# Kernel optimization log

Hardware: AMD Instinct MI355X
Metric: run time of the kernel (lower is better)

Reference implementation:

```python
import jax, jax.numpy as jnp
import numpy as np

B, C, O, H, W, K, KS = 32, 128, 128, 56, 56, 4, 3
EPS = 1e-5


def setup_inputs() -> dict:
    key = jax.random.key(0)
    ks = jax.random.split(key, 6)
    sc = lambda k, shape, s: jax.random.normal(k, shape, jnp.float32) * s
    return {
        "x": jax.random.normal(ks[0], (B, C, H, W), jnp.float32),
        "fc1_w": sc(ks[1], (K, C), 0.05),
        "fc1_b": jnp.zeros((K,), jnp.float32),
        "fc2_w": sc(ks[2], (K, K), 0.3),
        "fc2_b": jnp.zeros((K,), jnp.float32),
        "weight": sc(ks[3], (K, O, C, KS, KS), 0.05),  # [K, out, in/groups, kh, kw]
        "bias": sc(ks[4], (K, O), 0.05),
        "gamma": jnp.ones((O,), jnp.float32),
        "beta": jnp.zeros((O,), jnp.float32),
    }


def reference(x, fc1_w, fc1_b, fc2_w, fc2_b, weight, bias, gamma, beta):
    # attention2d: global avg pool -> 1x1 conv (== linear) -> relu -> 1x1 conv -> softmax over K
    pooled = x.mean(axis=(2, 3))                          # [B, C]
    h = jax.nn.relu(pooled @ fc1_w.T + fc1_b)             # [B, K]
    attn = jax.nn.softmax(h @ fc2_w.T + fc2_b, axis=-1)   # [B, K]

    # per-sample aggregated kernel / bias
    agg_w = jnp.einsum('bk,koihw->boihw', attn, weight)   # [B, O, C, KS, KS]
    agg_b = attn @ bias                                    # [B, O]

    # per-sample conv (== groups=batch trick in torch)
    def conv_one(xi, wi):
        return jax.lax.conv_general_dilated(
            xi[None], wi, window_strides=(1, 1),
            padding=((1, 1), (1, 1)),
            dimension_numbers=('NCHW', 'OIHW', 'NCHW'))[0]

    out = jax.vmap(conv_one)(x, agg_w) + agg_b[:, :, None, None]  # [B, O, H, W]

    # BatchNorm2d in training mode: biased batch stats over (N, H, W)
    mean = out.mean(axis=(0, 2, 3))
    var = out.var(axis=(0, 2, 3))
    out = (out - mean[None, :, None, None]) * jax.lax.rsqrt(var + EPS)[None, :, None, None]
    out = out * gamma[None, :, None, None] + beta[None, :, None, None]
    return jax.nn.relu(out)
```

## Files before the change

### kernel.cpp

```cpp
#include <hip/hip_runtime.h>
#include <hip/hip_bf16.h>

#define BB 32
#define CC 128
#define OO 128
#define HH 56
#define WW 56
#define KK 4
#define HW 3136
#define WPLANE 147456
#define EPSV 1e-5f

#define NPOS 348
#define BUFB 22528

typedef __attribute__((ext_vector_type(8))) short short8v;
typedef __attribute__((ext_vector_type(4))) float f32x4;

static __device__ __forceinline__ void gload16(const void* g, void* l) {
    __builtin_amdgcn_global_load_lds((const __attribute__((address_space(1))) void*)g,
                                     (__attribute__((address_space(3))) void*)l, 16, 0, 0);
}

__global__ void convert_pool_kernel(const float* __restrict__ x,
                                    ushort* __restrict__ xbf,
                                    float* __restrict__ pooledp,
                                    ushort* __restrict__ zpage) {
    const int h = blockIdx.x, b = blockIdx.y;
    if (h == 0 && b == 0 && threadIdx.x < 32) zpage[threadIdx.x] = 0;
    __shared__ float4 xl4[1792];
    const float* xp = x + (size_t)(b * CC) * HW + h * WW;

    #pragma unroll
    for (int k = 0; k < 7; ++k) {
        int u = threadIdx.x + k * 256;
        int c = u / 14, w4 = u - c * 14;
        float4 v = *(const float4*)(xp + (size_t)c * HW + w4 * 4);
        xl4[u ^ ((c >> 3) & 7)] = v;
    }
    __syncthreads();

    const float* xf = (const float*)xl4;
    #pragma unroll
    for (int k = 0; k < 4; ++k) {
        int v = threadIdx.x + k * 256;
        if (v < 896) {
            int w = v >> 4, c8 = v & 15;
            int w4 = w >> 2, wo = w & 3;
            short8v res;
            #pragma unroll
            for (int j = 0; j < 8; ++j) {
                int c = c8 * 8 + j;
                int su = (c * 14 + w4) ^ (c8 & 7);
                __hip_bfloat16 hb = __float2bfloat16(xf[su * 4 + wo]);
                res[j] = *(short*)&hb;
            }
            *(short8v*)(xbf + ((size_t)((b * HH + h) * WW + w)) * CC + c8 * 8) = res;
        }
    }

    if (threadIdx.x < 128) {
        int c = threadIdx.x;
        float s = 0.f;
        #pragma unroll
        for (int w4 = 0; w4 < 14; ++w4) {
            float4 v = xl4[(c * 14 + w4) ^ ((c >> 3) & 7)];
            s += v.x + v.y + v.z + v.w;
        }
        pooledp[((size_t)(b * HH + h)) * CC + c] = s;
    }
}

__global__ void attn_kernel(const float* __restrict__ pooledp,
                            const float* __restrict__ fc1_w, const float* __restrict__ fc1_b,
                            const float* __restrict__ fc2_w, const float* __restrict__ fc2_b,
                            float* __restrict__ attn) {
    const int b = blockIdx.x, c = threadIdx.x;
    float s = 0.f;
    for (int h = 0; h < HH; ++h) s += pooledp[((size_t)(b * HH + h)) * CC + c];
    const float pc = s * (1.0f / HW);
    __shared__ float red[8];
    const int lane = c & 63, wid = c >> 6;
    #pragma unroll
    for (int k = 0; k < KK; ++k) {
        float v = pc * fc1_w[k * CC + c];
        for (int off = 32; off > 0; off >>= 1) v += __shfl_down(v, off, 64);
        if (lane == 0) red[k * 2 + wid] = v;
    }
    __syncthreads();
    if (c == 0) {
        float hk[KK], z[KK], m = -1e30f, den = 0.f;
        #pragma unroll
        for (int k = 0; k < KK; ++k)
            hk[k] = fmaxf(red[k * 2] + red[k * 2 + 1] + fc1_b[k], 0.f);
        #pragma unroll
        for (int k = 0; k < KK; ++k) {
            float t = fc2_b[k];
            #pragma unroll
            for (int j = 0; j < KK; ++j) t += hk[j] * fc2_w[k * KK + j];
            z[k] = t; m = fmaxf(m, t);
        }
        #pragma unroll
        for (int k = 0; k < KK; ++k) { z[k] = expf(z[k] - m); den += z[k]; }
        #pragma unroll
        for (int k = 0; k < KK; ++k) attn[b * KK + k] = z[k] / den;
    }
}

__global__ void aggw_kernel(const float* __restrict__ attn, const float* __restrict__ weight,
                            const float* __restrict__ bias,
                            ushort* __restrict__ aggw, float* __restrict__ agg_b) {
    int idx = blockIdx.x * 256 + threadIdx.x;
    if (idx < BB * 9 * OO * CC) {
        int cc = idx & 31;
        int t1 = idx >> 5;
        int o  = t1 & 127;
        int t2 = t1 >> 7;
        int ci = t2 & 3;
        int t3 = t2 >> 2;
        int j  = t3 % 9;
        int b  = t3 / 9;
        int c  = ci * 32 + cc;
        size_t wi = ((size_t)(o * CC + c)) * 9 + j;
        float s = attn[b*KK + 0] * weight[wi]
                + attn[b*KK + 1] * weight[wi + (size_t)WPLANE]
                + attn[b*KK + 2] * weight[wi + (size_t)2*WPLANE]
                + attn[b*KK + 3] * weight[wi + (size_t)3*WPLANE];
        __hip_bfloat16 hb = __float2bfloat16(s);
        aggw[idx] = *(ushort*)&hb;
    }
    if (blockIdx.x < 16) {
        int i = blockIdx.x * 256 + threadIdx.x;
        int b = i >> 7, o = i & 127;
        float s = 0.f;
        #pragma unroll
        for (int k = 0; k < KK; ++k) s += attn[b*KK + k] * bias[k*OO + o];
        agg_b[i] = s;
    }
}

static __device__ __forceinline__ void conv_body(
        const ushort* __restrict__ xbf, const ushort* __restrict__ aggw,
        const ushort* __restrict__ zpage, ushort* xs,
        int b, int h0, int wg, int wy, int cf, int kg, int wid, int lane,
        f32x4 (&acc)[4][7]) {
    const ushort* gp[6]; int gstep[6];
    #pragma unroll
    for (int k = 0; k < 6; ++k) {
        int q = wid + 4 * k;
        int un = q * 64 + lane;
        int u = un ^ ((un >> 3) & 7);
        int pos = u >> 2, quad = u & 3;
        int row = pos / 58, col = pos - row * 58;
        int gh = h0 - 1 + row, gw = col - 1;
        bool valid = (pos < NPOS) && (gh >= 0) && (gh < HH) && (gw >= 0) && (gw < WW);
        gp[k] = valid ? (xbf + ((size_t)((b * HH + gh) * WW + gw)) * CC + quad * 8) : zpage;
        gstep[k] = valid ? 32 : 0;
    }

    int blin[7];
    #pragma unroll
    for (int nf = 0; nf < 7; ++nf) {
        int p = wy * 112 + nf * 16 + cf;
        int r = p / 56, w = p - r * 56;
        blin[nf] = (((r + 1) * 58 + (w + 1)) << 6) + kg * 16;
    }

    const ushort* Ab = aggw + ((size_t)b * 36) * 4096 + (size_t)(wg * 64 + cf) * 32 + kg * 8;
    #define ALOAD(mf_, j_, ci_) (*(const short8v*)(Ab + (size_t)((j_) * 4 + (ci_)) * 4096 + (mf_) * 512))

    short8v pa[4];
    #pragma unroll
    for (int mf = 0; mf < 4; ++mf) pa[mf] = ALOAD(mf, 0, 0);

    #pragma unroll
    for (int k = 0; k < 6; ++k) {
        int q = wid + 4 * k;
        if (q < 22) { gload16(gp[k], (char*)xs + q * 1024); gp[k] += gstep[k]; }
    }
    __syncthreads();

    int cur = 0;
    for (int ci = 0; ci < 4; ++ci) {
        if (ci < 3) {
            char* base = (char*)xs + (cur ^ 1) * BUFB;
            #pragma unroll
            for (int k = 0; k < 6; ++k) {
                int q = wid + 4 * k;
                if (q < 22) { gload16(gp[k], base + q * 1024); gp[k] += gstep[k]; }
            }
        }
        const char* xbuf = (const char*)xs + cur * BUFB;

        short8v bfc[7], bfn[7];
        #pragma unroll
        for (int nf = 0; nf < 7; ++nf) {
            int lin = blin[nf] + (-58 - 1) * 64;
            int swz = lin ^ ((lin >> 3) & 0x70);
            bfc[nf] = *(const short8v*)(xbuf + swz);
        }
        #pragma unroll
        for (int j = 0; j < 9; ++j) {
            if (j < 8) {
                const int toff = (((j+1)/3 - 1) * 58 + ((j+1)%3 - 1)) * 64;
                #pragma unroll
                for (int nf = 0; nf < 7; ++nf) {
                    int lin = blin[nf] + toff;
                    int swz = lin ^ ((lin >> 3) & 0x70);
                    bfn[nf] = *(const short8v*)(xbuf + swz);
                }
            }
            short8v ca[4];
            #pragma unroll
            for (int mf = 0; mf < 4; ++mf) ca[mf] = pa[mf];
            if (j < 8) {
                #pragma unroll
                for (int mf = 0; mf < 4; ++mf) pa[mf] = ALOAD(mf, j + 1, ci);
            } else if (ci < 3) {
                #pragma unroll
                for (int mf = 0; mf < 4; ++mf) pa[mf] = ALOAD(mf, 0, ci + 1);
            }
            #pragma unroll
            for (int nf = 0; nf < 7; ++nf) {
                #pragma unroll
                for (int mf = 0; mf < 4; ++mf)
                    acc[mf][nf] = __builtin_amdgcn_mfma_f32_16x16x32_bf16(ca[mf], bfc[nf], acc[mf][nf], 0, 0, 0);
            }
            if (j < 8) {
                #pragma unroll
                for (int nf = 0; nf < 7; ++nf) bfc[nf] = bfn[nf];
            }
        }
        if (ci < 3) __syncthreads();
        cur ^= 1;
    }
    #undef ALOAD
}

template <bool BF16OUT>
__launch_bounds__(256, 2)
__global__ void conv_kernel(const ushort* __restrict__ xbf, const ushort* __restrict__ aggw,
                            const float* __restrict__ agg_b, const ushort* __restrict__ zpage,
                            void* __restrict__ outv,
                            float* __restrict__ psum, float* __restrict__ psumsq) {
    const int lid  = blockIdx.x;
    const int gwid = (lid & 7) * 56 + (lid >> 3);
    const int b = gwid / 14;
    const int t = gwid - b * 14;
    const int h0 = t * 4;
    __shared__ ushort xs[2 * BUFB / 2];

    const int tid  = threadIdx.x;
    const int lane = tid & 63;
    const int wid  = tid >> 6;
    const int wg = wid & 1, wy = wid >> 1;
    const int cf = lane & 15, kg = lane >> 4;

    f32x4 acc[4][7];
    #pragma unroll
    for (int mf = 0; mf < 4; ++mf)
        #pragma unroll
        for (int nf = 0; nf < 7; ++nf) acc[mf][nf] = (f32x4){0.f, 0.f, 0.f, 0.f};

    conv_body(xbf, aggw, zpage, xs, b, h0, wg, wy, cf, kg, wid, lane, acc);

    #pragma unroll
    for (int mf = 0; mf < 4; ++mf) {
        #pragma unroll
        for (int i = 0; i < 4; ++i) {
            const int o = wg * 64 + mf * 16 + kg * 4 + i;
            const float ab = agg_b[b * OO + o];
            const size_t obase = ((size_t)(b * OO + o)) * HW;
            float s = 0.f, s2 = 0.f;
            #pragma unroll
            for (int nf = 0; nf < 7; ++nf) {
                int p = wy * 112 + nf * 16 + cf;
                int r = p / 56, w = p - r * 56;
                float v = acc[mf][nf][i] + ab;
                if (BF16OUT) {
                    __hip_bfloat16 hb = __float2bfloat16(v);
                    ((ushort*)outv)[obase + (h0 + r) * WW + w] = *(ushort*)&hb;
                } else {
                    ((float*)outv)[obase + (h0 + r) * WW + w] = v;
                }
                s += v; s2 += v * v;
            }
            s  += __shfl_xor(s, 1, 64);  s  += __shfl_xor(s, 2, 64);
            s  += __shfl_xor(s, 4, 64);  s  += __shfl_xor(s, 8, 64);
            s2 += __shfl_xor(s2, 1, 64); s2 += __shfl_xor(s2, 2, 64);
            s2 += __shfl_xor(s2, 4, 64); s2 += __shfl_xor(s2, 8, 64);
            if (cf == 0) {
                int row = (b * 14 + t) * 2 + wy;
                psum[row * OO + o]   = s;
                psumsq[row * OO + o] = s2;
            }
        }
    }
}

__global__ void finstats_kernel(const float* __restrict__ psum, const float* __restrict__ psumsq,
                                float* __restrict__ sums, float* __restrict__ sumsq) {
    const int o = blockIdx.x, l = threadIdx.x;
    float s = 0.f, s2 = 0.f;
    for (int r = l; r < 896; r += 64) { s += psum[r * OO + o]; s2 += psumsq[r * OO + o]; }
    for (int off = 32; off > 0; off >>= 1) {
        s  += __shfl_down(s, off, 64);
        s2 += __shfl_down(s2, off, 64);
    }
    if (l == 0) { sums[o] = s; sumsq[o] = s2; }
}

__global__ void bn_bf16_kernel(const ushort* __restrict__ convout, float* __restrict__ out,
                               const float* __restrict__ sums, const float* __restrict__ sumsq,
                               const float* __restrict__ gamma, const float* __restrict__ beta) {
    const float invN = 1.0f / (float)(BB * HW);
    const int total8 = BB * OO * HW / 8;
    for (int i = blockIdx.x * blockDim.x + threadIdx.x; i < total8; i += gridDim.x * blockDim.x) {
        int o = (i / (HW/8)) % OO;
        float mean = sums[o] * invN;
        float var  = sumsq[o] * invN - mean*mean;
        float inv  = rsqrtf(var + EPSV);
        float g  = gamma[o] * inv;
        float bt = beta[o] - mean * g;
        short8v v = *(const short8v*)(convout + (size_t)i * 8);
        float4 lo, hi;
        #pragma unroll
        for (int j = 0; j < 4; ++j) {
            ushort u = (ushort)v[j];
            float f = __bfloat162float(*(__hip_bfloat16*)&u);
            ((float*)&lo)[j] = fmaxf(f * g + bt, 0.f);
        }
        #pragma unroll
        for (int j = 0; j < 4; ++j) {
            ushort u = (ushort)v[4 + j];
            float f = __bfloat162float(*(__hip_bfloat16*)&u);
            ((float*)&hi)[j] = fmaxf(f * g + bt, 0.f);
        }
        ((float4*)out)[i * 2]     = lo;
        ((float4*)out)[i * 2 + 1] = hi;
    }
}

__global__ void bn_kernel(float* __restrict__ out,
                          const float* __restrict__ sums, const float* __restrict__ sumsq,
                          const float* __restrict__ gamma, const float* __restrict__ beta) {
    const float invN = 1.0f / (float)(BB * HW);
    const int total4 = BB * OO * HW / 4;
    for (int i = blockIdx.x * blockDim.x + threadIdx.x; i < total4; i += gridDim.x * blockDim.x) {
        int o = (i / (HW/4)) % OO;
        float mean = sums[o] * invN;
        float var  = sumsq[o] * invN - mean*mean;
        float inv  = rsqrtf(var + EPSV);
        float g  = gamma[o] * inv;
        float bt = beta[o] - mean * g;
        float4 v = ((float4*)out)[i];
        v.x = fmaxf(v.x*g + bt, 0.f);
        v.y = fmaxf(v.y*g + bt, 0.f);
        v.z = fmaxf(v.z*g + bt, 0.f);
        v.w = fmaxf(v.w*g + bt, 0.f);
        ((float4*)out)[i] = v;
    }
}

extern "C" void kernel_launch(void* const* d_in, const int* in_sizes, int n_in,
                              void* d_out, int out_size, void* d_ws, size_t ws_size,
                              hipStream_t stream) {
    const float* x      = (const float*)d_in[0];
    const float* fc1_w  = (const float*)d_in[1];
    const float* fc1_b  = (const float*)d_in[2];
    const float* fc2_w  = (const float*)d_in[3];
    const float* fc2_b  = (const float*)d_in[4];
    const float* weight = (const float*)d_in[5];
    const float* bias   = (const float*)d_in[6];
    const float* gamma  = (const float*)d_in[7];
    const float* beta   = (const float*)d_in[8];
    float* out = (float*)d_out;

    const size_t XBF_ELEMS  = (size_t)BB * HW * CC;
    const size_t AGGW_ELEMS = (size_t)BB * 9 * OO * CC;
    const size_t OUT_ELEMS  = (size_t)BB * OO * HW;
    ushort* xbf  = (ushort*)d_ws;
    ushort* aggw = xbf + XBF_ELEMS;
    float*  wsf  = (float*)(aggw + AGGW_ELEMS);
    float* pooledp = wsf;
    float* attn    = pooledp + 229376;
    float* agg_b   = attn + 128;
    float* psum    = agg_b + 4096;
    float* psumsq  = psum + 114688;
    float* sums    = psumsq + 114688;
    float* sumsq   = sums + 128;
    ushort* zpage  = (ushort*)(sumsq + 128);
    ushort* convout = (ushort*)(zpage + 32);

    const size_t need = (size_t)((char*)(convout + OUT_ELEMS) - (char*)d_ws);
    const bool bf16path = ws_size >= need;

    convert_pool_kernel<<<dim3(HH, BB), 256, 0, stream>>>(x, xbf, pooledp, zpage);
    attn_kernel<<<BB, 128, 0, stream>>>(pooledp, fc1_w, fc1_b, fc2_w, fc2_b, attn);
    aggw_kernel<<<(int)((AGGW_ELEMS + 255)/256), 256, 0, stream>>>(attn, weight, bias, aggw, agg_b);

    if (bf16path) {
        conv_kernel<true><<<dim3(448), 256, 0, stream>>>(xbf, aggw, agg_b, zpage,
                                                         (void*)convout, psum, psumsq);
        finstats_kernel<<<OO, 64, 0, stream>>>(psum, psumsq, sums, sumsq);
        bn_bf16_kernel<<<2048, 256, 0, stream>>>(convout, out, sums, sumsq, gamma, beta);
    } else {
        conv_kernel<false><<<dim3(448), 256, 0, stream>>>(xbf, aggw, agg_b, zpage,
                                                          (void*)out, psum, psumsq);
        finstats_kernel<<<OO, 64, 0, stream>>>(psum, psumsq, sums, sumsq);
        bn_kernel<<<2048, 256, 0, stream>>>(out, sums, sumsq, gamma, beta);
    }
}
```

Baseline: 99.77 us.

## Fuse attention into aggw, fold BN stats into apply kernel, deepen weight prefetch

Merges the attention MLP kernel into the aggregated-weight kernel, so every block recomputes the per-sample attention from the pooled partial sums. The stats-finalise kernel is merged into a per-channel BN apply kernel, and the partial sums are transposed to a channel-major layout so each block reads them contiguously. The conv inner loop now prefetches aggregated-weight fragments two taps ahead instead of one. Together these remove two kernel launches and hide more global latency, at the cost of redundant attention and stats reductions per block and more registers in the conv kernel.

```diff
diff --git a/kernel.cpp b/kernel.cpp
--- a/kernel.cpp
+++ b/kernel.cpp
@@ -71,24 +71,35 @@
     }
 }
 
-__global__ void attn_kernel(const float* __restrict__ pooledp,
-                            const float* __restrict__ fc1_w, const float* __restrict__ fc1_b,
-                            const float* __restrict__ fc2_w, const float* __restrict__ fc2_b,
-                            float* __restrict__ attn) {
-    const int b = blockIdx.x, c = threadIdx.x;
-    float s = 0.f;
-    for (int h = 0; h < HH; ++h) s += pooledp[((size_t)(b * HH + h)) * CC + c];
-    const float pc = s * (1.0f / HW);
+__global__ void attn_aggw_kernel(const float* __restrict__ pooledp,
+                                 const float* __restrict__ fc1_w, const float* __restrict__ fc1_b,
+                                 const float* __restrict__ fc2_w, const float* __restrict__ fc2_b,
+                                 const float* __restrict__ weight, const float* __restrict__ bias,
+                                 ushort* __restrict__ aggw, float* __restrict__ agg_b) {
+    const int b   = blockIdx.x / 36;
+    const int rem = blockIdx.x % 36;
+    const int j   = rem >> 2;
+    const int ci  = rem & 3;
+
     __shared__ float red[8];
-    const int lane = c & 63, wid = c >> 6;
-    #pragma unroll
-    for (int k = 0; k < KK; ++k) {
-        float v = pc * fc1_w[k * CC + c];
-        for (int off = 32; off > 0; off >>= 1) v += __shfl_down(v, off, 64);
-        if (lane == 0) red[k * 2 + wid] = v;
-    }
-    __syncthreads();
-    if (c == 0) {
+    __shared__ float att[4];
+    const int tid = threadIdx.x;
+    const int lane = tid & 63, wv = tid >> 6;
+
+    if (tid < 128) {
+        const int c = tid;
+        float s = 0.f;
+        for (int h = 0; h < HH; ++h) s += pooledp[((size_t)(b * HH + h)) * CC + c];
+        const float pc = s * (1.0f / HW);
+        #pragma unroll
+        for (int k = 0; k < KK; ++k) {
+            float v = pc * fc1_w[k * CC + c];
+            for (int off = 32; off > 0; off >>= 1) v += __shfl_down(v, off, 64);
+            if (lane == 0) red[k * 2 + wv] = v;
+        }
+    }
+    __syncthreads();
+    if (tid == 0) {
         float hk[KK], z[KK], m = -1e30f, den = 0.f;
         #pragma unroll
         for (int k = 0; k < KK; ++k)
@@ -97,45 +108,38 @@
         for (int k = 0; k < KK; ++k) {
             float t = fc2_b[k];
             #pragma unroll
-            for (int j = 0; j < KK; ++j) t += hk[j] * fc2_w[k * KK + j];
+            for (int jj = 0; jj < KK; ++jj) t += hk[jj] * fc2_w[k * KK + jj];
             z[k] = t; m = fmaxf(m, t);
         }
         #pragma unroll
         for (int k = 0; k < KK; ++k) { z[k] = expf(z[k] - m); den += z[k]; }
         #pragma unroll
-        for (int k = 0; k < KK; ++k) attn[b * KK + k] = z[k] / den;
-    }
-}
-
-__global__ void aggw_kernel(const float* __restrict__ attn, const float* __restrict__ weight,
-                            const float* __restrict__ bias,
-                            ushort* __restrict__ aggw, float* __restrict__ agg_b) {
-    int idx = blockIdx.x * 256 + threadIdx.x;
-    if (idx < BB * 9 * OO * CC) {
-        int cc = idx & 31;
-        int t1 = idx >> 5;
-        int o  = t1 & 127;
-        int t2 = t1 >> 7;
-        int ci = t2 & 3;
-        int t3 = t2 >> 2;
-        int j  = t3 % 9;
-        int b  = t3 / 9;
-        int c  = ci * 32 + cc;
+        for (int k = 0; k < KK; ++k) att[k] = z[k] / den;
+    }
+    __syncthreads();
+    const float a0 = att[0], a1 = att[1], a2 = att[2], a3 = att[3];
+
+    if (rem == 0 && tid < 128) {
+        const int o = tid;
+        float s = 0.f;
+        #pragma unroll
+        for (int k = 0; k < KK; ++k) s += att[k] * bias[k * OO + o];
+        agg_b[b * OO + o] = s;
+    }
+
+    ushort* op = aggw + (((size_t)b * 9 + j) * 4 + ci) * 4096;
+    #pragma unroll 4
+    for (int it = 0; it < 16; ++it) {
+        int idx2 = tid + it * 256;
+        int cc = idx2 & 31, o = idx2 >> 5;
+        int c = ci * 32 + cc;
         size_t wi = ((size_t)(o * CC + c)) * 9 + j;
-        float s = attn[b*KK + 0] * weight[wi]
-                + attn[b*KK + 1] * weight[wi + (size_t)WPLANE]
-                + attn[b*KK + 2] * weight[wi + (size_t)2*WPLANE]
-                + attn[b*KK + 3] * weight[wi + (size_t)3*WPLANE];
+        float s = a0 * weight[wi]
+                + a1 * weight[wi + (size_t)WPLANE]
+                + a2 * weight[wi + (size_t)2*WPLANE]
+                + a3 * weight[wi + (size_t)3*WPLANE];
         __hip_bfloat16 hb = __float2bfloat16(s);
-        aggw[idx] = *(ushort*)&hb;
-    }
-    if (blockIdx.x < 16) {
-        int i = blockIdx.x * 256 + threadIdx.x;
-        int b = i >> 7, o = i & 127;
-        float s = 0.f;
-        #pragma unroll
-        for (int k = 0; k < KK; ++k) s += attn[b*KK + k] * bias[k*OO + o];
-        agg_b[i] = s;
+        op[idx2] = *(ushort*)&hb;
     }
 }
 
@@ -169,9 +173,11 @@
     const ushort* Ab = aggw + ((size_t)b * 36) * 4096 + (size_t)(wg * 64 + cf) * 32 + kg * 8;
     #define ALOAD(mf_, j_, ci_) (*(const short8v*)(Ab + (size_t)((j_) * 4 + (ci_)) * 4096 + (mf_) * 512))
 
-    short8v pa[4];
-    #pragma unroll
-    for (int mf = 0; mf < 4; ++mf) pa[mf] = ALOAD(mf, 0, 0);
+    short8v paA[4], paB[4];
+    #pragma unroll
+    for (int mf = 0; mf < 4; ++mf) paA[mf] = ALOAD(mf, 0, 0);
+    #pragma unroll
+    for (int mf = 0; mf < 4; ++mf) paB[mf] = ALOAD(mf, 1, 0);
 
     #pragma unroll
     for (int k = 0; k < 6; ++k) {
@@ -212,13 +218,14 @@
             }
             short8v ca[4];
             #pragma unroll
-            for (int mf = 0; mf < 4; ++mf) ca[mf] = pa[mf];
-            if (j < 8) {
-                #pragma unroll
-                for (int mf = 0; mf < 4; ++mf) pa[mf] = ALOAD(mf, j + 1, ci);
+            for (int mf = 0; mf < 4; ++mf) { ca[mf] = paA[mf]; paA[mf] = paB[mf]; }
+            const int f = j + 2;
+            if (f < 9) {
+                #pragma unroll
+                for (int mf = 0; mf < 4; ++mf) paB[mf] = ALOAD(mf, f, ci);
             } else if (ci < 3) {
                 #pragma unroll
-                for (int mf = 0; mf < 4; ++mf) pa[mf] = ALOAD(mf, 0, ci + 1);
+                for (int mf = 0; mf < 4; ++mf) paB[mf] = ALOAD(mf, f - 9, ci + 1);
             }
             #pragma unroll
             for (int nf = 0; nf < 7; ++nf) {
@@ -291,74 +298,77 @@
             s2 += __shfl_xor(s2, 4, 64); s2 += __shfl_xor(s2, 8, 64);
             if (cf == 0) {
                 int row = (b * 14 + t) * 2 + wy;
-                psum[row * OO + o]   = s;
-                psumsq[row * OO + o] = s2;
-            }
-        }
-    }
-}
-
-__global__ void finstats_kernel(const float* __restrict__ psum, const float* __restrict__ psumsq,
-                                float* __restrict__ sums, float* __restrict__ sumsq) {
-    const int o = blockIdx.x, l = threadIdx.x;
+                psum[o * 896 + row]   = s;
+                psumsq[o * 896 + row] = s2;
+            }
+        }
+    }
+}
+
+template <bool BF16IN>
+__global__ void bn2_kernel(const void* __restrict__ src, float* __restrict__ out,
+                           const float* __restrict__ psum, const float* __restrict__ psumsq,
+                           const float* __restrict__ gamma, const float* __restrict__ beta) {
+    const int o  = blockIdx.x & 127;
+    const int bg = blockIdx.x >> 7;
+    const int tid = threadIdx.x;
+    const int lane = tid & 63, wv = tid >> 6;
+    __shared__ float red[8];
+    __shared__ float par[2];
+
     float s = 0.f, s2 = 0.f;
-    for (int r = l; r < 896; r += 64) { s += psum[r * OO + o]; s2 += psumsq[r * OO + o]; }
+    for (int r = tid; r < 896; r += 256) {
+        s  += psum[o * 896 + r];
+        s2 += psumsq[o * 896 + r];
+    }
     for (int off = 32; off > 0; off >>= 1) {
         s  += __shfl_down(s, off, 64);
         s2 += __shfl_down(s2, off, 64);
     }
-    if (l == 0) { sums[o] = s; sumsq[o] = s2; }
-}
-
-__global__ void bn_bf16_kernel(const ushort* __restrict__ convout, float* __restrict__ out,
-                               const float* __restrict__ sums, const float* __restrict__ sumsq,
-                               const float* __restrict__ gamma, const float* __restrict__ beta) {
-    const float invN = 1.0f / (float)(BB * HW);
-    const int total8 = BB * OO * HW / 8;
-    for (int i = blockIdx.x * blockDim.x + threadIdx.x; i < total8; i += gridDim.x * blockDim.x) {
-        int o = (i / (HW/8)) % OO;
-        float mean = sums[o] * invN;
-        float var  = sumsq[o] * invN - mean*mean;
+    if (lane == 0) { red[wv] = s; red[4 + wv] = s2; }
+    __syncthreads();
+    if (tid == 0) {
+        const float invN = 1.0f / (float)(BB * HW);
+        float S  = red[0] + red[1] + red[2] + red[3];
+        float S2 = red[4] + red[5] + red[6] + red[7];
+        float mean = S * invN;
+        float var  = S2 * invN - mean * mean;
         float inv  = rsqrtf(var + EPSV);
-        float g  = gamma[o] * inv;
-        float bt = beta[o] - mean * g;
-        short8v v = *(const short8v*)(convout + (size_t)i * 8);
-        float4 lo, hi;
-        #pragma unroll
-        for (int j = 0; j < 4; ++j) {
-            ushort u = (ushort)v[j];
-            float f = __bfloat162float(*(__hip_bfloat16*)&u);
-            ((float*)&lo)[j] = fmaxf(f * g + bt, 0.f);
-        }
-        #pragma unroll
-        for (int j = 0; j < 4; ++j) {
-            ushort u = (ushort)v[4 + j];
-            float f = __bfloat162float(*(__hip_bfloat16*)&u);
-            ((float*)&hi)[j] = fmaxf(f * g + bt, 0.f);
-        }
-        ((float4*)out)[i * 2]     = lo;
-        ((float4*)out)[i * 2 + 1] = hi;
-    }
-}
-
-__global__ void bn_kernel(float* __restrict__ out,
-                          const float* __restrict__ sums, const float* __restrict__ sumsq,
-                          const float* __restrict__ gamma, const float* __restrict__ beta) {
-    const float invN = 1.0f / (float)(BB * HW);
-    const int total4 = BB * OO * HW / 4;
-    for (int i = blockIdx.x * blockDim.x + threadIdx.x; i < total4; i += gridDim.x * blockDim.x) {
-        int o = (i / (HW/4)) % OO;
-        float mean = sums[o] * invN;
-        float var  = sumsq[o] * invN - mean*mean;
-        float inv  = rsqrtf(var + EPSV);
-        float g  = gamma[o] * inv;
-        float bt = beta[o] - mean * g;
-        float4 v = ((float4*)out)[i];
-        v.x = fmaxf(v.x*g + bt, 0.f);
-        v.y = fmaxf(v.y*g + bt, 0.f);
-        v.z = fmaxf(v.z*g + bt, 0.f);
-        v.w = fmaxf(v.w*g + bt, 0.f);
-        ((float4*)out)[i] = v;
+        par[0] = gamma[o] * inv;
+        par[1] = beta[o] - mean * par[0];
+    }
+    __syncthreads();
+    const float g = par[0], bt = par[1];
+
+    #pragma unroll
+    for (int b2 = 0; b2 < 4; ++b2) {
+        const int b = bg * 4 + b2;
+        const size_t base = ((size_t)(b * OO + o)) * HW;
+        for (int u = tid; u < 392; u += 256) {
+            float4 lo, hi;
+            if (BF16IN) {
+                short8v v = *(const short8v*)((const ushort*)src + base + u * 8);
+                #pragma unroll
+                for (int jj = 0; jj < 4; ++jj) {
+                    ushort uu = (ushort)v[jj];
+                    ((float*)&lo)[jj] = fmaxf(__bfloat162float(*(__hip_bfloat16*)&uu) * g + bt, 0.f);
+                }
+                #pragma unroll
+                for (int jj = 0; jj < 4; ++jj) {
+                    ushort uu = (ushort)v[4 + jj];
+                    ((float*)&hi)[jj] = fmaxf(__bfloat162float(*(__hip_bfloat16*)&uu) * g + bt, 0.f);
+                }
+            } else {
+                float4 v0 = *(const float4*)((const float*)src + base + u * 8);
+                float4 v1 = *(const float4*)((const float*)src + base + u * 8 + 4);
+                lo.x = fmaxf(v0.x * g + bt, 0.f); lo.y = fmaxf(v0.y * g + bt, 0.f);
+                lo.z = fmaxf(v0.z * g + bt, 0.f); lo.w = fmaxf(v0.w * g + bt, 0.f);
+                hi.x = fmaxf(v1.x * g + bt, 0.f); hi.y = fmaxf(v1.y * g + bt, 0.f);
+                hi.z = fmaxf(v1.z * g + bt, 0.f); hi.w = fmaxf(v1.w * g + bt, 0.f);
+            }
+            *(float4*)(out + base + u * 8)     = lo;
+            *(float4*)(out + base + u * 8 + 4) = hi;
+        }
     }
 }
 
@@ -396,18 +406,17 @@
     const bool bf16path = ws_size >= need;
 
     convert_pool_kernel<<<dim3(HH, BB), 256, 0, stream>>>(x, xbf, pooledp, zpage);
-    attn_kernel<<<BB, 128, 0, stream>>>(pooledp, fc1_w, fc1_b, fc2_w, fc2_b, attn);
-    aggw_kernel<<<(int)((AGGW_ELEMS + 255)/256), 256, 0, stream>>>(attn, weight, bias, aggw, agg_b);
-
+    attn_aggw_kernel<<<dim3(1152), 256, 0, stream>>>(pooledp, fc1_w, fc1_b, fc2_w, fc2_b,
+                                                     weight, bias, aggw, agg_b);
     if (bf16path) {
         conv_kernel<true><<<dim3(448), 256, 0, stream>>>(xbf, aggw, agg_b, zpage,
                                                          (void*)convout, psum, psumsq);
-        finstats_kernel<<<OO, 64, 0, stream>>>(psum, psumsq, sums, sumsq);
-        bn_bf16_kernel<<<2048, 256, 0, stream>>>(convout, out, sums, sumsq, gamma, beta);
+        bn2_kernel<true><<<dim3(1024), 256, 0, stream>>>((const void*)convout, out,
+                                                         psum, psumsq, gamma, beta);
     } else {
         conv_kernel<false><<<dim3(448), 256, 0, stream>>>(xbf, aggw, agg_b, zpage,
                                                           (void*)out, psum, psumsq);
-        finstats_kernel<<<OO, 64, 0, stream>>>(psum, psumsq, sums, sumsq);
-        bn_kernel<<<2048, 256, 0, stream>>>(out, sums, sumsq, gamma, beta);
-    }
-}
+        bn2_kernel<false><<<dim3(1024), 256, 0, stream>>>((const void*)out, out,
+                                                          psum, psumsq, gamma, beta);
+    }
+}
```

Result: slower. 105.2 us (+5.5%).
